# Kernel tuning notes

Hardware: AMD Instinct MI355X
Metric: run time of the kernel (lower is better)

## Reference

```python
import jax, jax.numpy as jnp
import numpy as np

P_FACTOR = 3.0
EPS = 1e-12  # torch F.normalize eps


def _l2norm(x):
    # F.normalize(x, dim=1): divide by max(||x||_2, eps) along feature dim
    n = jnp.sqrt(jnp.sum(x * x, axis=1, keepdims=True))
    return x / jnp.maximum(n, EPS)


def setup_inputs() -> dict:
    key = jax.random.key(0)
    ks = jax.random.split(key, 7)
    B, N, F, E = 4096, 20000, 768, 512
    X = jax.random.normal(ks[0], (B, F), jnp.float32)
    D = jax.random.normal(ks[1], (N, F), jnp.float32)
    r = jax.random.uniform(ks[2], (N, 1), jnp.float32)  # correctness in [0,1]
    g_w = jax.random.normal(ks[3], (E, F), jnp.float32) * (1.0 / np.sqrt(F))
    g_b = jax.random.normal(ks[4], (E,), jnp.float32) * 0.01
    h_w = jax.random.normal(ks[5], (1, 1), jnp.float32)
    h_b = jax.random.normal(ks[6], (1,), jnp.float32) * 0.01
    return {"X": X, "D": D, "r": r, "g_w": g_w, "g_b": g_b, "h_w": h_w, "h_b": h_b}


def reference(X, D, r, g_w, g_b, h_w, h_b):
    # register_buffer path: r = ex_correct * 2 - 1
    r = r * 2.0 - 1.0
    # g: Linear(feat_dim -> feat_embed_dim) on both queries and exemplars
    Xe = X @ g_w.T + g_b            # [B, E]
    De = D @ g_w.T + g_b            # [N, E]
    # h: Linear(1 -> class_embed_dim)
    rh = r @ h_w.T + h_b            # [N, C]
    # Minerva: cosine similarity -> power-law activation -> weighted retrieval
    a = _l2norm(Xe) @ _l2norm(De).T                 # [B, N]
    a = jnp.sign(a) * jnp.abs(a) ** P_FACTOR        # |s|^p * sign(s)
    logits = a @ rh                                 # [B, C]
    preds = jax.nn.sigmoid(logits)
    return logits, preds
```

## Files before the change

kernel.cpp:

```cpp
#include <hip/hip_runtime.h>
#include <cstdint>


typedef __attribute__((ext_vector_type(4))) float  f32x4;
typedef __attribute__((ext_vector_type(8))) __bf16 bf16x8;
typedef __attribute__((ext_vector_type(4))) __bf16 bf16x4;

constexpr int B = 4096, N = 20000, F = 768, E = 512;

#define AS1CAST(p) ((__attribute__((address_space(1))) unsigned int*)(uintptr_t)(p))
#define AS3CAST(p) ((__attribute__((address_space(3))) unsigned int*)(uintptr_t)(p))

__device__ __forceinline__ void gload_lds16(const void* g, void* l) {
  __builtin_amdgcn_global_load_lds(AS1CAST(g), AS3CAST(l), 16, 0, 0);
}


__global__ void k_prep(const float* __restrict__ X, const float* __restrict__ D,
                       const float* __restrict__ G, const float* __restrict__ r,
                       const float* __restrict__ hw, const float* __restrict__ hb,
                       __bf16* __restrict__ Xb, __bf16* __restrict__ Db,
                       __bf16* __restrict__ Gb, float* __restrict__ rh,
                       float* __restrict__ lg, float* __restrict__ norm2) {
  const int t = blockIdx.x * blockDim.x + threadIdx.x;
  const int stride = gridDim.x * blockDim.x;
  constexpr int nX = B * F / 4, nD = N * F / 4, nG = E * F / 4;
  constexpr int tot = nX + nD + nG;
  for (int i = t; i < tot; i += stride) {
    const float4* src; bf16x4* dst; int off;
    if (i < nX)           { src = (const float4*)X; dst = (bf16x4*)Xb; off = i; }
    else if (i < nX + nD) { src = (const float4*)D; dst = (bf16x4*)Db; off = i - nX; }
    else                  { src = (const float4*)G; dst = (bf16x4*)Gb; off = i - nX - nD; }
    float4 v = src[off];
    bf16x4 o;
    o[0] = (__bf16)v.x; o[1] = (__bf16)v.y; o[2] = (__bf16)v.z; o[3] = (__bf16)v.w;
    dst[off] = o;
  }
  if (t < N) rh[t] = (2.0f * r[t] - 1.0f) * hw[0] + hb[0];
  if (t < B) lg[t] = 0.0f;
  if (t < B + N) norm2[t] = 0.0f;
}


__global__ __launch_bounds__(256, 3)
void k_embed(const __bf16* __restrict__ Xb, const __bf16* __restrict__ Db,
             const __bf16* __restrict__ Gb, const float* __restrict__ bias,
             __bf16* __restrict__ Eb, float* __restrict__ norm2) {
  constexpr int K = F;
  __shared__ __bf16 As[128 * 64];
  __shared__ __bf16 Bs[128 * 64];
  __shared__ float ssum[128];
  const int tid  = threadIdx.x;
  const int wave = tid >> 6;
  const int lane = tid & 63;
  const int by = blockIdx.y;
  const bool isX = (by < B / 128);
  const __bf16* A = isX ? Xb : Db;
  const int m0 = isX ? by * 128 : (by - B / 128) * 128;
  const int Mr = isX ? B : N;
  const int g0 = by * 128;
  const int n0 = blockIdx.x * 128;
  if (tid < 128) ssum[tid] = 0.0f;

  const int srow = tid >> 3;
  const int scg  = (tid & 7) ^ (srow & 7);
  const __bf16* ga[4];
  const __bf16* gb[4];
  __bf16* la[4];
  __bf16* lb[4];
#pragma unroll
  for (int q = 0; q < 4; ++q) {
    const int row = srow + q * 32;
    int arow = m0 + row; if (arow >= Mr) arow = Mr - 1;
    const int brow = n0 + row;
    ga[q] = A  + (size_t)arow * K + scg * 8;
    gb[q] = Gb + (size_t)brow * K + scg * 8;
    la[q] = &As[q * 2048 + tid * 8];
    lb[q] = &Bs[q * 2048 + tid * 8];
  }

  const int mw = (wave & 1) * 64;
  const int nw = (wave >> 1) * 64;
  const int quad = lane >> 4;
  const int l15  = lane & 15;
  f32x4 acc[4][4] = {};

  for (int kb = 0; kb < K; kb += 64) {
#pragma unroll
    for (int q = 0; q < 4; ++q) gload_lds16(ga[q] + kb, la[q]);
#pragma unroll
    for (int q = 0; q < 4; ++q) gload_lds16(gb[q] + kb, lb[q]);
    __syncthreads();
#pragma unroll
    for (int h = 0; h < 2; ++h) {
      bf16x8 af[4], bfr[4];
#pragma unroll
      for (int i = 0; i < 4; ++i) {
        const int rr = mw + i * 16 + l15;
        af[i] = *(const bf16x8*)&As[rr * 64 + ((quad + h * 4) ^ (rr & 7)) * 8];
      }
#pragma unroll
      for (int j = 0; j < 4; ++j) {
        const int rr = nw + j * 16 + l15;
        bfr[j] = *(const bf16x8*)&Bs[rr * 64 + ((quad + h * 4) ^ (rr & 7)) * 8];
      }
#pragma unroll
      for (int i = 0; i < 4; ++i)
#pragma unroll
        for (int j = 0; j < 4; ++j)
          acc[i][j] = __builtin_amdgcn_mfma_f32_16x16x32_bf16(af[i], bfr[j], acc[i][j], 0, 0, 0);
    }
    __syncthreads();
  }

#pragma unroll
  for (int i = 0; i < 4; ++i) {
    float part[4] = {0.0f, 0.0f, 0.0f, 0.0f};
#pragma unroll
    for (int j = 0; j < 4; ++j) {
      const int col = n0 + nw + j * 16 + l15;
      const float bv = bias[col];
#pragma unroll
      for (int rr = 0; rr < 4; ++rr) {
        const int row = mw + i * 16 + quad * 4 + rr;
        if (m0 + row < Mr) {
          const __bf16 hv = (__bf16)(acc[i][j][rr] + bv);
          Eb[(size_t)(g0 + row) * E + col] = hv;
          const float vb = (float)hv;
          part[rr] += vb * vb;
        }
      }
    }
#pragma unroll
    for (int rr = 0; rr < 4; ++rr) {
      float v = part[rr];
      v += __shfl_xor(v, 1);
      v += __shfl_xor(v, 2);
      v += __shfl_xor(v, 4);
      v += __shfl_xor(v, 8);
      if (l15 == 0) atomicAdd(&ssum[mw + i * 16 + quad * 4 + rr], v);
    }
  }
  __syncthreads();
  if (tid < 128 && m0 + tid < Mr) atomicAdd(&norm2[g0 + tid], ssum[tid]);
}


__global__ __launch_bounds__(256, 3)
void k_minerva(const __bf16* __restrict__ Xe, const __bf16* __restrict__ De,
               const float* __restrict__ norm2, const float* __restrict__ rh,
               float* __restrict__ logits) {
  constexpr int K  = 512;
  constexpr int MT = B / 128;
  constexpr int NT = (N + 127) / 128;
  constexpr int W  = 20;
  __shared__ __bf16 As[128 * 64];
  __shared__ __bf16 Bs[128 * 64];
  __shared__ float lsum[128];
  const int tid  = threadIdx.x;
  const int lane = tid & 63;
  const int wave = tid >> 6;

  const int bid   = blockIdx.x;
  const int panel = bid / (W * MT);
  const int bn    = panel * W;
  const int rem   = bid - panel * (W * MT);
  const int mt    = rem % MT;
  const int nt    = bn + rem / MT;
  const int m0 = mt * 128, n0 = nt * 128;
  if (tid < 128) lsum[tid] = 0.0f;

  const int srow = tid >> 3;
  const int scg  = (tid & 7) ^ (srow & 7);
  const __bf16* ga[4];
  const __bf16* gb[4];
  __bf16* la[4];
  __bf16* lb[4];
#pragma unroll
  for (int q = 0; q < 4; ++q) {
    const int row = srow + q * 32;
    const int arow = m0 + row;
    int brow = n0 + row; if (brow >= N) brow = N - 1;
    ga[q] = Xe + (size_t)arow * K + scg * 8;
    gb[q] = De + (size_t)brow * K + scg * 8;
    la[q] = &As[q * 2048 + tid * 8];
    lb[q] = &Bs[q * 2048 + tid * 8];
  }

  const int mw = (wave & 1) * 64;
  const int nw = (wave >> 1) * 64;
  const int quad = lane >> 4;
  const int l15  = lane & 15;
  f32x4 acc[4][4] = {};

  for (int kb = 0; kb < K; kb += 64) {
#pragma unroll
    for (int q = 0; q < 4; ++q) gload_lds16(ga[q] + kb, la[q]);
#pragma unroll
    for (int q = 0; q < 4; ++q) gload_lds16(gb[q] + kb, lb[q]);
    __syncthreads();
#pragma unroll
    for (int h = 0; h < 2; ++h) {
      bf16x8 af[4], bfr[4];
#pragma unroll
      for (int i = 0; i < 4; ++i) {
        const int rr = mw + i * 16 + l15;
        af[i] = *(const bf16x8*)&As[rr * 64 + ((quad + h * 4) ^ (rr & 7)) * 8];
      }
#pragma unroll
      for (int j = 0; j < 4; ++j) {
        const int rr = nw + j * 16 + l15;
        bfr[j] = *(const bf16x8*)&Bs[rr * 64 + ((quad + h * 4) ^ (rr & 7)) * 8];
      }
#pragma unroll
      for (int i = 0; i < 4; ++i)
#pragma unroll
        for (int j = 0; j < 4; ++j)
          acc[i][j] = __builtin_amdgcn_mfma_f32_16x16x32_bf16(af[i], bfr[j], acc[i][j], 0, 0, 0);
    }
    __syncthreads();
  }

  float id3rh[4];
#pragma unroll
  for (int j = 0; j < 4; ++j) {
    const int col = n0 + nw + j * 16 + l15;
    if (col < N) {
      const float id = 1.0f / fmaxf(sqrtf(norm2[B + col]), 1e-12f);
      id3rh[j] = id * id * id * rh[col];
    } else id3rh[j] = 0.0f;
  }
#pragma unroll
  for (int i = 0; i < 4; ++i) {
    float ix3[4];
#pragma unroll
    for (int rr = 0; rr < 4; ++rr) {
      const int row = m0 + mw + i * 16 + quad * 4 + rr;
      const float ix = 1.0f / fmaxf(sqrtf(norm2[row]), 1e-12f);
      ix3[rr] = ix * ix * ix;
    }
    float part[4] = {0.0f, 0.0f, 0.0f, 0.0f};
#pragma unroll
    for (int j = 0; j < 4; ++j)
#pragma unroll
      for (int rr = 0; rr < 4; ++rr) {
        const float a = acc[i][j][rr];
        const float a2 = a * a;
        part[rr] = fmaf(a2 * a, id3rh[j], part[rr]);
      }
#pragma unroll
    for (int rr = 0; rr < 4; ++rr) {
      float v = part[rr] * ix3[rr];
      v += __shfl_xor(v, 1);
      v += __shfl_xor(v, 2);
      v += __shfl_xor(v, 4);
      v += __shfl_xor(v, 8);
      if (l15 == 0) atomicAdd(&lsum[mw + i * 16 + quad * 4 + rr], v);
    }
  }
  __syncthreads();
  if (tid < 128) atomicAdd(&logits[m0 + tid], lsum[tid]);
}


__global__ void k_finalize(const float* __restrict__ logits, float* __restrict__ out, int n) {
  int i = blockIdx.x * blockDim.x + threadIdx.x;
  if (i < n) {
    float L = logits[i];
    out[i] = L;
    out[n + i] = 1.0f / (1.0f + expf(-L));
  }
}


extern "C" void kernel_launch(void* const* d_in, const int* in_sizes, int n_in,
                              void* d_out, int out_size, void* d_ws, size_t ws_size,
                              hipStream_t stream) {
  const float* X   = (const float*)d_in[0];
  const float* D   = (const float*)d_in[1];
  const float* r   = (const float*)d_in[2];
  const float* g_w = (const float*)d_in[3];
  const float* g_b = (const float*)d_in[4];
  const float* h_w = (const float*)d_in[5];
  const float* h_b = (const float*)d_in[6];
  float* out = (float*)d_out;

  char* ws = (char*)d_ws;
  __bf16* Xb    = (__bf16*)(ws + 0);
  __bf16* Db    = (__bf16*)(ws + 6291456);
  __bf16* Gb    = (__bf16*)(ws + 37011456);
  __bf16* Eb    = (__bf16*)(ws + 37797888);
  float*  rh    = (float*) (ws + 62472192);
  float*  norm2 = (float*) (ws + 62552192);
  float*  lg    = (float*) (ws + 62648576);

  k_prep<<<2048, 256, 0, stream>>>(X, D, g_w, r, h_w, h_b, Xb, Db, Gb, rh, lg, norm2);

  k_embed<<<dim3(E / 128, B / 128 + (N + 127) / 128), 256, 0, stream>>>(
      Xb, Db, Gb, g_b, Eb, norm2);

  k_minerva<<<157 * 32, 256, 0, stream>>>(Eb, Eb + (size_t)B * E, norm2, rh, lg);

  k_finalize<<<(B + 255) / 256, 256, 0, stream>>>(lg, out, B);
}
```

Measured before the change: 251.5 us.

## Restructure minerva GEMM into 256x256 double-buffered tiles with 8-wave ping-pong

Changes the similarity GEMM kernel from 128x128 tiles with 4 waves and one LDS buffer to 256x256 tiles with 8 waves, double-buffered LDS, and loads for the next k-step interleaved between four MFMA quadrant phases. It uses s_setprio and explicit vmcnt waits to overlap global-to-LDS copies with matrix math. It also swaps the panel block swizzle for an XCD-aware mapping. The aim is more data reuse per loaded byte and hidden load latency, at the cost of 128KB LDS, more registers, and more barriers.

```diff
diff --git a/kernel.cpp b/kernel.cpp
--- a/kernel.cpp
+++ b/kernel.cpp
@@ -146,96 +146,177 @@
 }
 
 
-__global__ __launch_bounds__(256, 3)
+__global__ __launch_bounds__(512, 2)
 void k_minerva(const __bf16* __restrict__ Xe, const __bf16* __restrict__ De,
                const float* __restrict__ norm2, const float* __restrict__ rh,
                float* __restrict__ logits) {
-  constexpr int K  = 512;
-  constexpr int MT = B / 128;
-  constexpr int NT = (N + 127) / 128;
-  constexpr int W  = 20;
-  __shared__ __bf16 As[128 * 64];
-  __shared__ __bf16 Bs[128 * 64];
-  __shared__ float lsum[128];
-  const int tid  = threadIdx.x;
-  const int lane = tid & 63;
-  const int wave = tid >> 6;
-
-  const int bid   = blockIdx.x;
-  const int panel = bid / (W * MT);
-  const int bn    = panel * W;
-  const int rem   = bid - panel * (W * MT);
-  const int mt    = rem % MT;
-  const int nt    = bn + rem / MT;
-  const int m0 = mt * 128, n0 = nt * 128;
-  if (tid < 128) lsum[tid] = 0.0f;
-
-  const int srow = tid >> 3;
-  const int scg  = (tid & 7) ^ (srow & 7);
-  const __bf16* ga[4];
-  const __bf16* gb[4];
-  __bf16* la[4];
-  __bf16* lb[4];
-#pragma unroll
-  for (int q = 0; q < 4; ++q) {
-    const int row = srow + q * 32;
-    const int arow = m0 + row;
-    int brow = n0 + row; if (brow >= N) brow = N - 1;
-    ga[q] = Xe + (size_t)arow * K + scg * 8;
-    gb[q] = De + (size_t)brow * K + scg * 8;
-    la[q] = &As[q * 2048 + tid * 8];
-    lb[q] = &Bs[q * 2048 + tid * 8];
-  }
-
-  const int mw = (wave & 1) * 64;
-  const int nw = (wave >> 1) * 64;
-  const int quad = lane >> 4;
-  const int l15  = lane & 15;
-  f32x4 acc[4][4] = {};
-
-  for (int kb = 0; kb < K; kb += 64) {
-#pragma unroll
-    for (int q = 0; q < 4; ++q) gload_lds16(ga[q] + kb, la[q]);
-#pragma unroll
-    for (int q = 0; q < 4; ++q) gload_lds16(gb[q] + kb, lb[q]);
-    __syncthreads();
-#pragma unroll
-    for (int h = 0; h < 2; ++h) {
-      bf16x8 af[4], bfr[4];
-#pragma unroll
-      for (int i = 0; i < 4; ++i) {
-        const int rr = mw + i * 16 + l15;
-        af[i] = *(const bf16x8*)&As[rr * 64 + ((quad + h * 4) ^ (rr & 7)) * 8];
-      }
-#pragma unroll
-      for (int j = 0; j < 4; ++j) {
-        const int rr = nw + j * 16 + l15;
-        bfr[j] = *(const bf16x8*)&Bs[rr * 64 + ((quad + h * 4) ^ (rr & 7)) * 8];
-      }
-#pragma unroll
-      for (int i = 0; i < 4; ++i)
-#pragma unroll
-        for (int j = 0; j < 4; ++j)
-          acc[i][j] = __builtin_amdgcn_mfma_f32_16x16x32_bf16(af[i], bfr[j], acc[i][j], 0, 0, 0);
-    }
-    __syncthreads();
-  }
+  constexpr int K   = 512;
+  constexpr int NKT = K / 64;
+  constexpr int MT  = B / 256;
+  constexpr int NT  = (N + 255) / 256;
+  __shared__ __bf16 As[2][2][128 * 64];
+  __shared__ __bf16 Bs[2][2][128 * 64];
+  __shared__ float lsum[256];
+
+  const int tid   = threadIdx.x;
+  const int wave  = tid >> 6;
+  const int lane  = tid & 63;
+  const int quad  = lane >> 4;
+  const int l15   = lane & 15;
+  const int mwave = (wave >> 2) * 128;
+  const int nwave = (wave & 3) * 64;
+  const int ahalf = mwave >> 7;
+  const int bhalf = nwave >> 7;
+  const int brow0 = nwave & 64;
+
+  const int wg = (blockIdx.x & 7) * (MT * NT / 8) + (blockIdx.x >> 3);
+  const int m0 = (wg & (MT - 1)) * 256;
+  const int n0 = (wg >> 4) * 256;
+
+  if (tid < 256) lsum[tid] = 0.0f;
+
+  const char* XeB = (const char*)Xe;
+  const char* DeB = (const char*)De;
+  unsigned offA[2][2], offB[2][2];
+#pragma unroll
+  for (int q = 0; q < 2; ++q) {
+    const int u  = q * 512 + tid;
+    const int r  = u >> 3;
+    const int cg = (u & 7) ^ (r & 7);
+#pragma unroll
+    for (int hf = 0; hf < 2; ++hf) {
+      offA[hf][q] = (unsigned)(m0 + hf * 128 + r) * (K * 2) + cg * 16;
+      int br = n0 + hf * 128 + r; if (br >= N) br = N - 1;
+      offB[hf][q] = (unsigned)br * (K * 2) + cg * 16;
+    }
+  }
+  const int ldsu = wave * 64 * 8;
+
+#define STAGE_A(kt, hf) do {                                              \
+    const int ktc_ = (((kt) < NKT) ? (kt) : (NKT - 1)) * 128;             \
+    __bf16* d_ = &As[(kt) & 1][hf][0];                                    \
+    gload_lds16(XeB + offA[hf][0] + ktc_, d_ + ldsu);                     \
+    gload_lds16(XeB + offA[hf][1] + ktc_, d_ + 4096 + ldsu);              \
+  } while (0)
+#define STAGE_B(kt, hf) do {                                              \
+    const int ktc_ = (((kt) < NKT) ? (kt) : (NKT - 1)) * 128;             \
+    __bf16* d_ = &Bs[(kt) & 1][hf][0];                                    \
+    gload_lds16(DeB + offB[hf][0] + ktc_, d_ + ldsu);                     \
+    gload_lds16(DeB + offB[hf][1] + ktc_, d_ + 4096 + ldsu);              \
+  } while (0)
+
+  STAGE_A(0, 0); STAGE_A(0, 1); STAGE_B(0, 0); STAGE_B(0, 1);
+  STAGE_A(1, 0); STAGE_A(1, 1);
+  asm volatile("s_waitcnt vmcnt(4)" ::: "memory");
+  __builtin_amdgcn_s_barrier();
+
+  f32x4 acc[8][4] = {};
+
+  for (int t = 0; t < NKT; ++t) {
+    const __bf16* Ab = &As[t & 1][ahalf][0];
+    const __bf16* Bb = &Bs[t & 1][bhalf][0];
+    bf16x8 a_lo[4][2], a_hi[4][2], b_lo[2][2], b_hi[2][2];
+
+#pragma unroll
+    for (int i = 0; i < 4; ++i) {
+      const int rr = i * 16 + l15;
+#pragma unroll
+      for (int h = 0; h < 2; ++h)
+        a_lo[i][h] = *(const bf16x8*)&Ab[rr * 64 + (((quad + h * 4) ^ (rr & 7)) * 8)];
+    }
+#pragma unroll
+    for (int j = 0; j < 2; ++j) {
+      const int rr = brow0 + j * 16 + l15;
+#pragma unroll
+      for (int h = 0; h < 2; ++h)
+        b_lo[j][h] = *(const bf16x8*)&Bb[rr * 64 + (((quad + h * 4) ^ (rr & 7)) * 8)];
+    }
+    STAGE_B(t + 1, 0);
+    __builtin_amdgcn_s_barrier();
+    __builtin_amdgcn_s_setprio(1);
+#pragma unroll
+    for (int h = 0; h < 2; ++h)
+#pragma unroll
+      for (int i = 0; i < 4; ++i)
+#pragma unroll
+        for (int j = 0; j < 2; ++j)
+          acc[i][j] = __builtin_amdgcn_mfma_f32_16x16x32_bf16(a_lo[i][h], b_lo[j][h], acc[i][j], 0, 0, 0);
+    __builtin_amdgcn_s_setprio(0);
+    __builtin_amdgcn_s_barrier();
+
+#pragma unroll
+    for (int i = 0; i < 4; ++i) {
+      const int rr = (i + 4) * 16 + l15;
+#pragma unroll
+      for (int h = 0; h < 2; ++h)
+        a_hi[i][h] = *(const bf16x8*)&Ab[rr * 64 + (((quad + h * 4) ^ (rr & 7)) * 8)];
+    }
+    STAGE_B(t + 1, 1);
+    __builtin_amdgcn_s_barrier();
+    __builtin_amdgcn_s_setprio(1);
+#pragma unroll
+    for (int h = 0; h < 2; ++h)
+#pragma unroll
+      for (int i = 0; i < 4; ++i)
+#pragma unroll
+        for (int j = 0; j < 2; ++j)
+          acc[i + 4][j] = __builtin_amdgcn_mfma_f32_16x16x32_bf16(a_hi[i][h], b_lo[j][h], acc[i + 4][j], 0, 0, 0);
+    __builtin_amdgcn_s_setprio(0);
+    __builtin_amdgcn_s_barrier();
+
+#pragma unroll
+    for (int j = 0; j < 2; ++j) {
+      const int rr = brow0 + (j + 2) * 16 + l15;
+#pragma unroll
+      for (int h = 0; h < 2; ++h)
+        b_hi[j][h] = *(const bf16x8*)&Bb[rr * 64 + (((quad + h * 4) ^ (rr & 7)) * 8)];
+    }
+    STAGE_A(t + 2, 0);
+    __builtin_amdgcn_s_barrier();
+    __builtin_amdgcn_s_setprio(1);
+#pragma unroll
+    for (int h = 0; h < 2; ++h)
+#pragma unroll
+      for (int i = 0; i < 4; ++i)
+#pragma unroll
+        for (int j = 0; j < 2; ++j)
+          acc[i][j + 2] = __builtin_amdgcn_mfma_f32_16x16x32_bf16(a_lo[i][h], b_hi[j][h], acc[i][j + 2], 0, 0, 0);
+    __builtin_amdgcn_s_setprio(0);
+    __builtin_amdgcn_s_barrier();
+
+    STAGE_A(t + 2, 1);
+    __builtin_amdgcn_s_barrier();
+    __builtin_amdgcn_s_setprio(1);
+#pragma unroll
+    for (int h = 0; h < 2; ++h)
+#pragma unroll
+      for (int i = 0; i < 4; ++i)
+#pragma unroll
+        for (int j = 0; j < 2; ++j)
+          acc[i + 4][j + 2] = __builtin_amdgcn_mfma_f32_16x16x32_bf16(a_hi[i][h], b_hi[j][h], acc[i + 4][j + 2], 0, 0, 0);
+    __builtin_amdgcn_s_setprio(0);
+    asm volatile("s_waitcnt vmcnt(4)" ::: "memory");
+    __builtin_amdgcn_s_barrier();
+  }
+
+  asm volatile("s_waitcnt vmcnt(0)" ::: "memory");
+  __builtin_amdgcn_s_barrier();
 
   float id3rh[4];
 #pragma unroll
   for (int j = 0; j < 4; ++j) {
-    const int col = n0 + nw + j * 16 + l15;
+    const int col = n0 + nwave + j * 16 + l15;
     if (col < N) {
       const float id = 1.0f / fmaxf(sqrtf(norm2[B + col]), 1e-12f);
       id3rh[j] = id * id * id * rh[col];
     } else id3rh[j] = 0.0f;
   }
 #pragma unroll
-  for (int i = 0; i < 4; ++i) {
+  for (int i = 0; i < 8; ++i) {
     float ix3[4];
 #pragma unroll
     for (int rr = 0; rr < 4; ++rr) {
-      const int row = m0 + mw + i * 16 + quad * 4 + rr;
+      const int row = m0 + mwave + i * 16 + quad * 4 + rr;
       const float ix = 1.0f / fmaxf(sqrtf(norm2[row]), 1e-12f);
       ix3[rr] = ix * ix * ix;
     }
@@ -244,7 +325,7 @@
     for (int j = 0; j < 4; ++j)
 #pragma unroll
       for (int rr = 0; rr < 4; ++rr) {
-        const float a = acc[i][j][rr];
+        const float a  = acc[i][j][rr];
         const float a2 = a * a;
         part[rr] = fmaf(a2 * a, id3rh[j], part[rr]);
       }
@@ -255,11 +336,13 @@
       v += __shfl_xor(v, 2);
       v += __shfl_xor(v, 4);
       v += __shfl_xor(v, 8);
-      if (l15 == 0) atomicAdd(&lsum[mw + i * 16 + quad * 4 + rr], v);
+      if (l15 == 0) atomicAdd(&lsum[mwave + i * 16 + quad * 4 + rr], v);
     }
   }
   __syncthreads();
-  if (tid < 128) atomicAdd(&logits[m0 + tid], lsum[tid]);
+  if (tid < 256) atomicAdd(&logits[m0 + tid], lsum[tid]);
+#undef STAGE_A
+#undef STAGE_B
 }
 
 
@@ -299,7 +382,7 @@
   k_embed<<<dim3(E / 128, B / 128 + (N + 127) / 128), 256, 0, stream>>>(
       Xb, Db, Gb, g_b, Eb, norm2);
 
-  k_minerva<<<157 * 32, 256, 0, stream>>>(Eb, Eb + (size_t)B * E, norm2, rh, lg);
+  k_minerva<<<16 * 79, 512, 0, stream>>>(Eb, Eb + (size_t)B * E, norm2, rh, lg);
 
   k_finalize<<<(B + 255) / 256, 256, 0, stream>>>(lg, out, B);
 }
```

Result: slower. 281.7 us (+12.0%).

## Fuse fp32-to-bf16 conversion of X and D into the embedding GEMM

Applied to the files above, without the earlier changes.

Removes the separate pass that converted X and D to bf16 in workspace; k_prep now only converts the weight matrix. The embedding GEMM loads fp32 A tiles into registers, converts them and stores them to LDS. This saves a full read and write pass over the large inputs. In exchange, each A tile is read in fp32 by the four column blocks, and those loads no longer use the async global-to-LDS path, which can add latency.

```diff
diff --git a/kernel.cpp b/kernel.cpp
--- a/kernel.cpp
+++ b/kernel.cpp
@@ -16,25 +16,17 @@
 }
 
 
-__global__ void k_prep(const float* __restrict__ X, const float* __restrict__ D,
-                       const float* __restrict__ G, const float* __restrict__ r,
+__global__ void k_prep(const float* __restrict__ G, const float* __restrict__ r,
                        const float* __restrict__ hw, const float* __restrict__ hb,
-                       __bf16* __restrict__ Xb, __bf16* __restrict__ Db,
                        __bf16* __restrict__ Gb, float* __restrict__ rh,
                        float* __restrict__ lg, float* __restrict__ norm2) {
   const int t = blockIdx.x * blockDim.x + threadIdx.x;
-  const int stride = gridDim.x * blockDim.x;
-  constexpr int nX = B * F / 4, nD = N * F / 4, nG = E * F / 4;
-  constexpr int tot = nX + nD + nG;
-  for (int i = t; i < tot; i += stride) {
-    const float4* src; bf16x4* dst; int off;
-    if (i < nX)           { src = (const float4*)X; dst = (bf16x4*)Xb; off = i; }
-    else if (i < nX + nD) { src = (const float4*)D; dst = (bf16x4*)Db; off = i - nX; }
-    else                  { src = (const float4*)G; dst = (bf16x4*)Gb; off = i - nX - nD; }
-    float4 v = src[off];
+  constexpr int nG = E * F / 4;
+  if (t < nG) {
+    float4 v = ((const float4*)G)[t];
     bf16x4 o;
     o[0] = (__bf16)v.x; o[1] = (__bf16)v.y; o[2] = (__bf16)v.z; o[3] = (__bf16)v.w;
-    dst[off] = o;
+    ((bf16x4*)Gb)[t] = o;
   }
   if (t < N) rh[t] = (2.0f * r[t] - 1.0f) * hw[0] + hb[0];
   if (t < B) lg[t] = 0.0f;
@@ -43,7 +35,7 @@
 
 
 __global__ __launch_bounds__(256, 3)
-void k_embed(const __bf16* __restrict__ Xb, const __bf16* __restrict__ Db,
+void k_embed(const float* __restrict__ Xf, const float* __restrict__ Df,
              const __bf16* __restrict__ Gb, const float* __restrict__ bias,
              __bf16* __restrict__ Eb, float* __restrict__ norm2) {
   constexpr int K = F;
@@ -55,7 +47,7 @@
   const int lane = tid & 63;
   const int by = blockIdx.y;
   const bool isX = (by < B / 128);
-  const __bf16* A = isX ? Xb : Db;
+  const float* A = isX ? Xf : Df;
   const int m0 = isX ? by * 128 : (by - B / 128) * 128;
   const int Mr = isX ? B : N;
   const int g0 = by * 128;
@@ -64,7 +56,7 @@
 
   const int srow = tid >> 3;
   const int scg  = (tid & 7) ^ (srow & 7);
-  const __bf16* ga[4];
+  const float*  ga[4];
   const __bf16* gb[4];
   __bf16* la[4];
   __bf16* lb[4];
@@ -87,9 +79,22 @@
 
   for (int kb = 0; kb < K; kb += 64) {
 #pragma unroll
-    for (int q = 0; q < 4; ++q) gload_lds16(ga[q] + kb, la[q]);
-#pragma unroll
     for (int q = 0; q < 4; ++q) gload_lds16(gb[q] + kb, lb[q]);
+    float4 av[4][2];
+#pragma unroll
+    for (int q = 0; q < 4; ++q) {
+      av[q][0] = *(const float4*)(ga[q] + kb);
+      av[q][1] = *(const float4*)(ga[q] + kb + 4);
+    }
+#pragma unroll
+    for (int q = 0; q < 4; ++q) {
+      bf16x8 o;
+      o[0] = (__bf16)av[q][0].x; o[1] = (__bf16)av[q][0].y;
+      o[2] = (__bf16)av[q][0].z; o[3] = (__bf16)av[q][0].w;
+      o[4] = (__bf16)av[q][1].x; o[5] = (__bf16)av[q][1].y;
+      o[6] = (__bf16)av[q][1].z; o[7] = (__bf16)av[q][1].w;
+      *(bf16x8*)la[q] = o;
+    }
     __syncthreads();
 #pragma unroll
     for (int h = 0; h < 2; ++h) {
@@ -286,18 +291,16 @@
   float* out = (float*)d_out;
 
   char* ws = (char*)d_ws;
-  __bf16* Xb    = (__bf16*)(ws + 0);
-  __bf16* Db    = (__bf16*)(ws + 6291456);
-  __bf16* Gb    = (__bf16*)(ws + 37011456);
-  __bf16* Eb    = (__bf16*)(ws + 37797888);
-  float*  rh    = (float*) (ws + 62472192);
-  float*  norm2 = (float*) (ws + 62552192);
-  float*  lg    = (float*) (ws + 62648576);
-
-  k_prep<<<2048, 256, 0, stream>>>(X, D, g_w, r, h_w, h_b, Xb, Db, Gb, rh, lg, norm2);
+  __bf16* Gb    = (__bf16*)(ws + 0);
+  __bf16* Eb    = (__bf16*)(ws + 786432);
+  float*  rh    = (float*) (ws + 25460736);
+  float*  norm2 = (float*) (ws + 25540736);
+  float*  lg    = (float*) (ws + 25637120);
+
+  k_prep<<<384, 256, 0, stream>>>(g_w, r, h_w, h_b, Gb, rh, lg, norm2);
 
   k_embed<<<dim3(E / 128, B / 128 + (N + 127) / 128), 256, 0, stream>>>(
-      Xb, Db, Gb, g_b, Eb, norm2);
+      X, D, Gb, g_b, Eb, norm2);
 
   k_minerva<<<157 * 32, 256, 0, stream>>>(Eb, Eb + (size_t)B * E, norm2, rh, lg);
 
```

New measurement: 269.6 us. 7.2% more time.
